# Kernel tuning notes

Measured on AMD Instinct MI355X. Metric: run time of the kernel, lower is better.

Reference implementation:

```python
import jax, jax.numpy as jnp
import numpy as np

B, T, D = 4, 2048, 1024
H = 16
DK = D // H


def setup_inputs() -> dict:
    key = jax.random.key(0)
    k1, k2, k3, k4 = jax.random.split(key, 4)
    x = jax.random.normal(k1, (B, T, D), dtype=jnp.float32)
    prefix_lengths = jax.random.randint(k2, (B,), 0, 1024, dtype=jnp.int64)
    # torch Linear weights: [out_features, in_features], scaled like kaiming-uniform-ish
    W_qkv = jax.random.normal(k3, (3 * D, D), dtype=jnp.float32) / np.sqrt(D)
    W_o = jax.random.normal(k4, (D, D), dtype=jnp.float32) / np.sqrt(D)
    return {"x": x, "prefix_lengths": prefix_lengths, "W_qkv": W_qkv, "W_o": W_o}


def _prefix_lm_mask(seq_len, prefix_lengths):
    # True where attention is BLOCKED.
    pos = jnp.arange(seq_len)
    key_pos = pos[None, None, :]          # [1,1,T]
    query_pos = pos[None, :, None]        # [1,T,1]
    prefix = prefix_lengths[:, None, None]  # [B,1,1]
    q_in_pre = query_pos < prefix
    k_in_pre = key_pos < prefix
    block_pre_to_suf = q_in_pre & ~k_in_pre
    block_future_suf = ~q_in_pre & ~k_in_pre & (key_pos > query_pos)
    return block_pre_to_suf | block_future_suf  # [B,T,T]


def reference(x, prefix_lengths, W_qkv, W_o):
    Bb, Tt, Cc = x.shape
    qkv = x @ W_qkv.T                     # [B,T,3D]
    qkv = qkv.reshape(Bb, Tt, 3, H, DK).transpose(2, 0, 3, 1, 4)  # [3,B,H,T,dk]
    q, k, v = qkv[0], qkv[1], qkv[2]
    scale = 1.0 / np.sqrt(DK).astype(np.float32)
    attn = jnp.einsum('bhqd,bhkd->bhqk', q, k) * scale  # [B,H,T,T]
    pl = jnp.clip(prefix_lengths.astype(jnp.int32), 0, Tt)
    mask = _prefix_lm_mask(Tt, pl)        # [B,T,T]
    attn = jnp.where(mask[:, None, :, :], -jnp.inf, attn)
    attn = jax.nn.softmax(attn, axis=-1)
    out = jnp.einsum('bhqk,bhkd->bhqd', attn, v)  # [B,H,T,dk]
    out = out.transpose(0, 2, 1, 3).reshape(Bb, Tt, Cc)
    return out @ W_o.T
```

## Files before the change

### kernel.cpp

```cpp
#include <hip/hip_runtime.h>
#include <stdint.h>

#define NB 4
#define NT 2048
#define ND 1024
#define NH 16
#define NDK 64
#define NTD 3072

typedef __attribute__((ext_vector_type(8))) short short8;
typedef __attribute__((ext_vector_type(4))) float f32x4;
typedef unsigned short u16;
typedef unsigned int u32;

__device__ __forceinline__ u16 f2bf(float f) {
    u32 u = __builtin_bit_cast(u32, f);
    u += 0x7fffu + ((u >> 16) & 1u);
    return (u16)(u >> 16);
}
__device__ __forceinline__ float bf2f(u16 s) {
    u32 u = ((u32)s) << 16;
    return __builtin_bit_cast(float, u);
}

__device__ __forceinline__ void gl_lds16(const u16* g, u16* l) {
    __builtin_amdgcn_global_load_lds(
        (const __attribute__((address_space(1))) u32*)g,
        (__attribute__((address_space(3))) u32*)l, 16, 0, 0);
}

__device__ __forceinline__ int swz(int row, int col) {
    return row * 32 + ((((col >> 3) ^ (row >> 1) ^ (row >> 3)) & 3) << 3) + (col & 7);
}

__global__ __launch_bounds__(256) void cvt_all(const float* __restrict__ x,
                                               const float* __restrict__ wqkv,
                                               const float* __restrict__ wo,
                                               u16* __restrict__ xb,
                                               u16* __restrict__ wqb,
                                               u16* __restrict__ wob) {
    const int n0 = NB * NT * ND;
    const int n1 = 3 * ND * ND;
    int i = (blockIdx.x * 256 + threadIdx.x) * 8;
    const float* src;
    u16* dst;
    if (i < n0) {
        src = x + i; dst = xb + i;
    } else if (i < n0 + n1) {
        src = wqkv + (i - n0); dst = wqb + (i - n0);
    } else {
        src = wo + (i - n0 - n1); dst = wob + (i - n0 - n1);
    }
    float4 a = *(const float4*)(src);
    float4 b = *(const float4*)(src + 4);
    short8 r;
    r[0] = (short)f2bf(a.x); r[1] = (short)f2bf(a.y);
    r[2] = (short)f2bf(a.z); r[3] = (short)f2bf(a.w);
    r[4] = (short)f2bf(b.x); r[5] = (short)f2bf(b.y);
    r[6] = (short)f2bf(b.z); r[7] = (short)f2bf(b.w);
    *(short8*)(dst) = r;
}

template <typename OutT>
__global__ __launch_bounds__(256) void gemm_bt(const u16* __restrict__ A,
                                               const u16* __restrict__ Bm,
                                               OutT* __restrict__ C,
                                               int M, int N, int K) {
    __shared__ __align__(16) u16 As[128 * 32];
    __shared__ __align__(16) u16 Bs[128 * 32];
    const int tid  = threadIdx.x;
    const int wave = tid >> 6, lane = tid & 63;
    const int quad = lane >> 4, l16 = lane & 15;
    const int wm = wave >> 1, wn = wave & 1;
    const int fid = blockIdx.y * gridDim.x + blockIdx.x;
    const int bx = ((fid & 7) << 3) | ((fid >> 3) & 7);
    const int by = fid >> 6;
    const int row0 = bx * 128, col0 = by * 128;

    f32x4 acc[4][4];
#pragma unroll
    for (int i = 0; i < 4; ++i)
#pragma unroll
        for (int j = 0; j < 4; ++j) acc[i][j] = (f32x4){0.f, 0.f, 0.f, 0.f};

    const u16* Ag = A + (size_t)(row0 + (tid >> 2)) * K + ((tid & 3) * 8);
    const u16* Bg = Bm + (size_t)(col0 + (tid >> 2)) * K + ((tid & 3) * 8);
    const size_t stride64 = (size_t)64 * K;
    u16* As0 = As + wave * 512;
    u16* As1 = As + 2048 + wave * 512;
    u16* Bs0 = Bs + wave * 512;
    u16* Bs1 = Bs + 2048 + wave * 512;

    for (int k0 = 0; k0 < K; k0 += 32) {
        gl_lds16(Ag + k0, As0);
        gl_lds16(Ag + k0 + stride64, As1);
        gl_lds16(Bg + k0, Bs0);
        gl_lds16(Bg + k0 + stride64, Bs1);
        __syncthreads();
        short8 af[4], bfr[4];
#pragma unroll
        for (int mi = 0; mi < 4; ++mi)
            af[mi] = *(const short8*)&As[(wm * 64 + mi * 16 + l16) * 32 + quad * 8];
#pragma unroll
        for (int ni = 0; ni < 4; ++ni)
            bfr[ni] = *(const short8*)&Bs[(wn * 64 + ni * 16 + l16) * 32 + quad * 8];
#pragma unroll
        for (int mi = 0; mi < 4; ++mi)
#pragma unroll
            for (int ni = 0; ni < 4; ++ni)
                acc[mi][ni] = __builtin_amdgcn_mfma_f32_16x16x32_bf16(
                    af[mi], bfr[ni], acc[mi][ni], 0, 0, 0);
        __syncthreads();
    }

#pragma unroll
    for (int mi = 0; mi < 4; ++mi) {
#pragma unroll
        for (int ni = 0; ni < 4; ++ni) {
            const int r = row0 + wm * 64 + mi * 16 + quad * 4;
            const int c = col0 + wn * 64 + ni * 16 + l16;
#pragma unroll
            for (int rr = 0; rr < 4; ++rr) {
                float v = acc[mi][ni][rr];
                if constexpr (sizeof(OutT) == 2)
                    C[(size_t)(r + rr) * N + c] = (OutT)f2bf(v);
                else
                    C[(size_t)(r + rr) * N + c] = (OutT)v;
            }
        }
    }
}

__global__ __launch_bounds__(256) void gemm_qkv(const u16* __restrict__ A,
                                                const u16* __restrict__ Bm,
                                                u16* __restrict__ Cq,
                                                u16* __restrict__ vtb) {
    const int Kd = ND, Nn = NTD;
    __shared__ __align__(16) u16 As[128 * 32];
    __shared__ __align__(16) u16 Bs[128 * 32];
    const int tid  = threadIdx.x;
    const int wave = tid >> 6, lane = tid & 63;
    const int quad = lane >> 4, l16 = lane & 15;
    const int wm = wave >> 1, wn = wave & 1;
    const int fid = blockIdx.y * gridDim.x + blockIdx.x;
    const int bx = ((fid & 7) << 3) | ((fid >> 3) & 7);
    const int by = fid >> 6;
    const int row0 = bx * 128, col0 = by * 128;

    f32x4 acc[4][4];
#pragma unroll
    for (int i = 0; i < 4; ++i)
#pragma unroll
        for (int j = 0; j < 4; ++j) acc[i][j] = (f32x4){0.f, 0.f, 0.f, 0.f};

    const u16* Ag = A + (size_t)(row0 + (tid >> 2)) * Kd + ((tid & 3) * 8);
    const u16* Bg = Bm + (size_t)(col0 + (tid >> 2)) * Kd + ((tid & 3) * 8);
    const size_t stride64 = (size_t)64 * Kd;
    u16* As0 = As + wave * 512;
    u16* As1 = As + 2048 + wave * 512;
    u16* Bs0 = Bs + wave * 512;
    u16* Bs1 = Bs + 2048 + wave * 512;

    for (int k0 = 0; k0 < Kd; k0 += 32) {
        gl_lds16(Ag + k0, As0);
        gl_lds16(Ag + k0 + stride64, As1);
        gl_lds16(Bg + k0, Bs0);
        gl_lds16(Bg + k0 + stride64, Bs1);
        __syncthreads();
        short8 af[4], bfr[4];
#pragma unroll
        for (int mi = 0; mi < 4; ++mi)
            af[mi] = *(const short8*)&As[(wm * 64 + mi * 16 + l16) * 32 + quad * 8];
#pragma unroll
        for (int ni = 0; ni < 4; ++ni)
            bfr[ni] = *(const short8*)&Bs[(wn * 64 + ni * 16 + l16) * 32 + quad * 8];
#pragma unroll
        for (int mi = 0; mi < 4; ++mi)
#pragma unroll
            for (int ni = 0; ni < 4; ++ni)
                acc[mi][ni] = __builtin_amdgcn_mfma_f32_16x16x32_bf16(
                    af[mi], bfr[ni], acc[mi][ni], 0, 0, 0);
        __syncthreads();
    }

    if (col0 < 2048) {
#pragma unroll
        for (int mi = 0; mi < 4; ++mi)
#pragma unroll
            for (int ni = 0; ni < 4; ++ni) {
                const int r = row0 + wm * 64 + mi * 16 + quad * 4;
                const int c = col0 + wn * 64 + ni * 16 + l16;
#pragma unroll
                for (int rr = 0; rr < 4; ++rr)
                    Cq[(size_t)(r + rr) * Nn + c] = f2bf(acc[mi][ni][rr]);
            }
    } else {
        const int hb = ((col0 - 2048) >> 6) + wn;
        const int bq = (row0 + wm * 64) >> 11;
        const int tb = (row0 + wm * 64) & 2047;
        u16* Ovt = vtb + (size_t)(bq * NH + hb) * 64 * NT + tb;
#pragma unroll
        for (int phase = 0; phase < 2; ++phase) {
            __syncthreads();
            if ((wave >> 1) == phase) {
                u16* L = (wave & 1) ? Bs : As;
#pragma unroll
                for (int mi = 0; mi < 4; ++mi) {
                    const int r4 = mi * 4 + quad;
#pragma unroll
                    for (int ni = 0; ni < 4; ++ni) {
                        const int cl = ni * 16 + l16;
                        u32 lo = (u32)f2bf(acc[mi][ni][0]) | ((u32)f2bf(acc[mi][ni][1]) << 16);
                        u32 hi = (u32)f2bf(acc[mi][ni][2]) | ((u32)f2bf(acc[mi][ni][3]) << 16);
                        u32* p = (u32*)&L[cl * 64 + (((r4 ^ cl) & 15) << 2)];
                        p[0] = lo; p[1] = hi;
                    }
                }
#pragma unroll
                for (int rep = 0; rep < 8; ++rep) {
                    const int cl = (lane >> 3) + rep * 8;
                    const int tc = lane & 7;
                    const u32* p0 = (const u32*)&L[cl * 64 + ((((2 * tc) ^ cl) & 15) << 2)];
                    const u32* p1 = (const u32*)&L[cl * 64 + ((((2 * tc + 1) ^ cl) & 15) << 2)];
                    u32 o0 = p0[0], o1 = p0[1], o2 = p1[0], o3 = p1[1];
                    u32* q = (u32*)(Ovt + (size_t)cl * NT + tc * 8);
                    q[0] = o0; q[1] = o1; q[2] = o2; q[3] = o3;
                }
            }
        }
    }
}

#define GETREG_XCC_ID 6164
__global__ __launch_bounds__(256) void flash_prefix(const u16* __restrict__ qkv,
                                                    const u16* __restrict__ vt,
                                                    const int* __restrict__ plen,
                                                    u16* __restrict__ attn,
                                                    u32* __restrict__ ctr) {
    __shared__ __align__(16) u16 Vt2[2][2048];
    __shared__ __align__(16) u16 Kt2[2][2048];
    __shared__ __align__(16) u16 Pl[4 * 512];
    __shared__ int taskS;

    const int tid  = threadIdx.x;
    const int wave = tid >> 6, lane = tid & 63;
    const int quad = lane >> 4, l16 = lane & 15;
    const float QSCALE = 0.18033688f;
    const int ldsoff = wave * 512;

    short8 ones;
#pragma unroll
    for (int j = 0; j < 8; ++j) ones[j] = (short)0x3F80;

    const bool is64 = (plen[1] == 0) && (plen[3] == 0);
    const int xcd = (int)(__builtin_amdgcn_s_getreg(GETREG_XCC_ID) & 7);
    int q = xcd;

    for (;;) {
        if (tid == 0) taskS = (int)atomicAdd(ctr + q * 16, 1u);
        __syncthreads();
        const int pos = taskS;
        if (pos >= 256) {
            q = (q + 1) & 7;
            if (q == xcd) break;
            continue;
        }

        const int bh = (q << 3) | (pos & 7);
        const int b = bh >> 4, h = bh & 15;
        const int q0 = (31 - (pos >> 3)) * 64;

        int P = is64 ? plen[2 * b] : plen[b];
        P = P < 0 ? 0 : (P > NT ? NT : P);

        const u16* Qg = qkv + (size_t)b * NT * NTD + h * NDK;
        const u16* Kg = Qg + ND;
        const u16* Vtb = vt + (size_t)bh * 64 * NT;
        const int qbase = q0 + wave * 16;
        u16* Pw = Pl + wave * 512;

        const int vrow = tid >> 2;
        const int vtq = (tid ^ (vrow >> 1) ^ (vrow >> 3)) & 3;
        const u16* vsrc = Vtb + (size_t)vrow * NT + vtq * 8;
        const int krow = tid >> 3;
        const int kc = (tid ^ krow) & 7;
        const u16* ksrc = Kg + (size_t)krow * NTD + kc * 8;

        short8 qa[2];
#pragma unroll
        for (int kd = 0; kd < 2; ++kd) {
            short8 tq = *(const short8*)(Qg + (size_t)(qbase + l16) * NTD + kd * 32 + quad * 8);
#pragma unroll
            for (int j = 0; j < 8; ++j)
                tq[j] = (short)f2bf(bf2f((u16)tq[j]) * QSCALE);
            qa[kd] = tq;
        }

        f32x4 o[4];
#pragma unroll
        for (int nt = 0; nt < 4; ++nt) o[nt] = (f32x4){0.f, 0.f, 0.f, 0.f};
        f32x4 lsum = (f32x4){0.f, 0.f, 0.f, 0.f};

        int kl[4];
#pragma unroll
        for (int rr = 0; rr < 4; ++rr) {
            const int qrow = qbase + quad * 4 + rr;
            kl[rr] = (qrow < P) ? P : (qrow + 1);
        }
        const int klmin = (qbase < P) ? P : (qbase + 1);
        const int kmax = (q0 + 64 > P) ? (q0 + 64) : P;

        gl_lds16(vsrc, &Vt2[0][ldsoff]);
        gl_lds16(ksrc, &Kt2[0][ldsoff]);
        int buf = 0;

        for (int k0 = 0; k0 < kmax; k0 += 32) {
            __syncthreads();
            if (k0 + 32 < kmax) {
                gl_lds16(vsrc + (k0 + 32), &Vt2[buf ^ 1][ldsoff]);
                gl_lds16(ksrc + (size_t)(k0 + 32) * NTD, &Kt2[buf ^ 1][ldsoff]);
            }
            const u16* Kb = Kt2[buf];
            const u16* Vb = Vt2[buf];

            f32x4 s[2];
#pragma unroll
            for (int ni = 0; ni < 2; ++ni) {
                s[ni] = (f32x4){0.f, 0.f, 0.f, 0.f};
#pragma unroll
                for (int kd = 0; kd < 2; ++kd) {
                    const int r = ni * 16 + l16;
                    const short8 kb = *(const short8*)&Kb[r * 64 + ((((kd * 4 + quad) ^ r) & 7) << 3)];
                    s[ni] = __builtin_amdgcn_mfma_f32_16x16x32_bf16(qa[kd], kb, s[ni], 0, 0, 0);
                }
            }

            const bool full = (k0 + 32 <= klmin);
#pragma unroll
            for (int ni = 0; ni < 2; ++ni) {
#pragma unroll
                for (int rr = 0; rr < 4; ++rr) {
                    float sv = s[ni][rr];
                    if (!full) {
                        const int kpos = k0 + ni * 16 + l16;
                        sv = (kpos < kl[rr]) ? sv : -1e30f;
                    }
                    const float p = exp2f(sv);
                    const u32 u = __builtin_bit_cast(u32, p) + 0x8000u;
                    Pw[swz(quad * 4 + rr, ni * 16 + l16)] = (u16)(u >> 16);
                }
            }

            const short8 pa = *(const short8*)&Pw[swz(l16, quad * 8)];
            lsum = __builtin_amdgcn_mfma_f32_16x16x32_bf16(pa, ones, lsum, 0, 0, 0);
#pragma unroll
            for (int nt = 0; nt < 4; ++nt) {
                const short8 vb = *(const short8*)&Vb[swz(nt * 16 + l16, quad * 8)];
                o[nt] = __builtin_amdgcn_mfma_f32_16x16x32_bf16(pa, vb, o[nt], 0, 0, 0);
            }
            buf ^= 1;
        }

#pragma unroll
        for (int rr = 0; rr < 4; ++rr) {
            const float inv = 1.0f / lsum[rr];
            const size_t rowoff = (size_t)(b * NT + qbase + quad * 4 + rr) * ND + h * NDK;
#pragma unroll
            for (int nt = 0; nt < 4; ++nt)
                attn[rowoff + nt * 16 + l16] = f2bf(o[nt][rr] * inv);
        }
    }
}

extern "C" void kernel_launch(void* const* d_in, const int* in_sizes, int n_in,
                              void* d_out, int out_size, void* d_ws, size_t ws_size,
                              hipStream_t stream) {
    const float* x    = (const float*)d_in[0];
    const int*   plen = (const int*)d_in[1];
    const float* wqkv = (const float*)d_in[2];
    const float* wo   = (const float*)d_in[3];
    float* out = (float*)d_out;

    char* ws = (char*)d_ws;
    u16* xb   = (u16*)(ws);
    u16* wqb  = (u16*)(ws + 16777216);
    u16* wob  = (u16*)(ws + 23068672);
    u16* qkv  = (u16*)(ws + 25165824);
    u16* attn = (u16*)(ws + 75497472);
    u16* vtb  = (u16*)(ws + 92274688);
    u32* ctr  = (u32*)(ws + 75496960);

    hipMemsetAsync(ctr, 0, 512, stream);

    cvt_all<<<6144, 256, 0, stream>>>(x, wqkv, wo, xb, wqb, wob);

    gemm_qkv<<<dim3(64, 24), 256, 0, stream>>>(xb, wqb, qkv, vtb);

    flash_prefix<<<1024, 256, 0, stream>>>(qkv, vtb, plen, attn, ctr);

    gemm_bt<float><<<dim3(64, 8), 256, 0, stream>>>(attn, wob, out, NB * NT, ND, ND);
}
```

Baseline: 297.8 us.

## Split QKV GEMM into 256x256 double-buffered QK kernel and separate V kernel

Splits the fused QKV projection in two. A new 512-thread kernel computes Q and K with 256x256 tiles, double-buffered LDS prefetch, XOR-swizzled LDS layout and MFMA priority hints. A separate 128x128 kernel computes V and writes it transposed. The larger tiles raise operand reuse and hide global load latency. The cost is an extra kernel launch and a smaller grid (256 blocks) for the QK part.

```diff
diff --git a/kernel.cpp b/kernel.cpp
--- a/kernel.cpp
+++ b/kernel.cpp
@@ -131,11 +131,119 @@
     }
 }
 
-__global__ __launch_bounds__(256) void gemm_qkv(const u16* __restrict__ A,
-                                                const u16* __restrict__ Bm,
-                                                u16* __restrict__ Cq,
-                                                u16* __restrict__ vtb) {
-    const int Kd = ND, Nn = NTD;
+__global__ __launch_bounds__(512, 2) void gemm_qk256(const u16* __restrict__ A,
+                                                     const u16* __restrict__ Bm,
+                                                     u16* __restrict__ Cq) {
+    __shared__ __align__(16) u16 rbA[2][8192];
+    __shared__ __align__(16) u16 rbB[2][8192];
+    u16* const rbAf = &rbA[0][0];
+    u16* const rbBf = &rbB[0][0];
+    const int tid  = threadIdx.x;
+    const int wave = tid >> 6, lane = tid & 63;
+    const int quad = lane >> 4, l16 = lane & 15;
+    const int wm = wave >> 2, wn = wave & 3;
+    const int K = ND;
+    const int fid = blockIdx.x;
+    const int bx = (fid & 7) * 4 + (fid >> 6);
+    const int by = (fid >> 3) & 7;
+    const int row0 = bx * 256, col0 = by * 256;
+
+    const int sr0 = tid >> 3, sl0 = (tid & 7) ^ (sr0 & 7);
+    const int a1 = 512 + tid;
+    const int sr1 = a1 >> 3, sl1 = (a1 & 7) ^ (sr1 & 7);
+    const int r0i = 2 * sr0 + (sl0 >> 2), k0i = (sl0 & 3) * 8;
+    const int r1i = 2 * sr1 + (sl1 >> 2), k1i = (sl1 & 3) * 8;
+    const u16* srcA0 = A + (size_t)(row0 + r0i) * K + k0i;
+    const u16* srcA1 = A + (size_t)(row0 + r1i) * K + k1i;
+    const u16* srcB0 = Bm + (size_t)(col0 + r0i) * K + k0i;
+    const u16* srcB1 = Bm + (size_t)(col0 + r1i) * K + k1i;
+    const int ldsc0 = wave * 512;
+    const int ldsc1 = 4096 + wave * 512;
+
+    int aoff[8], boff[4];
+#pragma unroll
+    for (int mi = 0; mi < 8; ++mi) {
+        const int row = wm * 128 + mi * 16 + l16;
+        const int srow = row >> 1;
+        const int slot = ((((row & 1) << 2) | quad) ^ (srow & 7));
+        aoff[mi] = srow * 64 + slot * 8;
+    }
+#pragma unroll
+    for (int ni = 0; ni < 4; ++ni) {
+        const int row = wn * 64 + ni * 16 + l16;
+        const int srow = row >> 1;
+        const int slot = ((((row & 1) << 2) | quad) ^ (srow & 7));
+        boff[ni] = srow * 64 + slot * 8;
+    }
+
+    f32x4 acc[8][4];
+#pragma unroll
+    for (int i = 0; i < 8; ++i)
+#pragma unroll
+        for (int j = 0; j < 4; ++j) acc[i][j] = (f32x4){0.f, 0.f, 0.f, 0.f};
+
+    gl_lds16(srcA0, rbAf + ldsc0);
+    gl_lds16(srcA1, rbAf + ldsc1);
+    gl_lds16(srcB0, rbBf + ldsc0);
+    gl_lds16(srcB1, rbBf + ldsc1);
+    __syncthreads();
+
+#define QK_TILE(T, TB, NB_)                                                    \
+    {                                                                          \
+        if ((T) + 1 < 32) {                                                    \
+            const int ko = ((T) + 1) * 32;                                     \
+            gl_lds16(srcA0 + ko, rbAf + (NB_) + ldsc0);                        \
+            gl_lds16(srcA1 + ko, rbAf + (NB_) + ldsc1);                        \
+            gl_lds16(srcB0 + ko, rbBf + (NB_) + ldsc0);                        \
+            gl_lds16(srcB1 + ko, rbBf + (NB_) + ldsc1);                        \
+        }                                                                      \
+        short8 af[4], bfr[4];                                                  \
+        _Pragma("unroll") for (int mi = 0; mi < 4; ++mi)                       \
+            af[mi] = *(const short8*)&rbAf[(TB) + aoff[mi]];                   \
+        _Pragma("unroll") for (int ni = 0; ni < 4; ++ni)                       \
+            bfr[ni] = *(const short8*)&rbBf[(TB) + boff[ni]];                  \
+        __builtin_amdgcn_s_setprio(1);                                         \
+        _Pragma("unroll") for (int mi = 0; mi < 4; ++mi)                       \
+            _Pragma("unroll") for (int ni = 0; ni < 4; ++ni)                   \
+                acc[mi][ni] = __builtin_amdgcn_mfma_f32_16x16x32_bf16(         \
+                    af[mi], bfr[ni], acc[mi][ni], 0, 0, 0);                    \
+        __builtin_amdgcn_s_setprio(0);                                         \
+        __builtin_amdgcn_s_barrier();                                          \
+        short8 af2[4];                                                         \
+        _Pragma("unroll") for (int mi = 0; mi < 4; ++mi)                       \
+            af2[mi] = *(const short8*)&rbAf[(TB) + aoff[4 + mi]];              \
+        __builtin_amdgcn_s_setprio(1);                                         \
+        _Pragma("unroll") for (int mi = 0; mi < 4; ++mi)                       \
+            _Pragma("unroll") for (int ni = 0; ni < 4; ++ni)                   \
+                acc[4 + mi][ni] = __builtin_amdgcn_mfma_f32_16x16x32_bf16(     \
+                    af2[mi], bfr[ni], acc[4 + mi][ni], 0, 0, 0);               \
+        __builtin_amdgcn_s_setprio(0);                                         \
+        __syncthreads();                                                       \
+    }
+
+    for (int t2 = 0; t2 < 32; t2 += 2) {
+        QK_TILE(t2, 0, 8192);
+        QK_TILE(t2 + 1, 8192, 0);
+    }
+#undef QK_TILE
+
+#pragma unroll
+    for (int mi = 0; mi < 8; ++mi) {
+#pragma unroll
+        for (int ni = 0; ni < 4; ++ni) {
+            const int r = row0 + wm * 128 + mi * 16 + quad * 4;
+            const int c = col0 + wn * 64 + ni * 16 + l16;
+#pragma unroll
+            for (int rr = 0; rr < 4; ++rr)
+                Cq[(size_t)(r + rr) * NTD + c] = f2bf(acc[mi][ni][rr]);
+        }
+    }
+}
+
+__global__ __launch_bounds__(256) void gemm_v(const u16* __restrict__ A,
+                                              const u16* __restrict__ Bm,
+                                              u16* __restrict__ vtb) {
+    const int Kd = ND;
     __shared__ __align__(16) u16 As[128 * 32];
     __shared__ __align__(16) u16 Bs[128 * 32];
     const int tid  = threadIdx.x;
@@ -145,7 +253,7 @@
     const int fid = blockIdx.y * gridDim.x + blockIdx.x;
     const int bx = ((fid & 7) << 3) | ((fid >> 3) & 7);
     const int by = fid >> 6;
-    const int row0 = bx * 128, col0 = by * 128;
+    const int row0 = bx * 128, col0 = 2048 + by * 128;
 
     f32x4 acc[4][4];
 #pragma unroll
@@ -183,49 +291,36 @@
         __syncthreads();
     }
 
-    if (col0 < 2048) {
-#pragma unroll
-        for (int mi = 0; mi < 4; ++mi)
-#pragma unroll
-            for (int ni = 0; ni < 4; ++ni) {
-                const int r = row0 + wm * 64 + mi * 16 + quad * 4;
-                const int c = col0 + wn * 64 + ni * 16 + l16;
-#pragma unroll
-                for (int rr = 0; rr < 4; ++rr)
-                    Cq[(size_t)(r + rr) * Nn + c] = f2bf(acc[mi][ni][rr]);
-            }
-    } else {
-        const int hb = ((col0 - 2048) >> 6) + wn;
-        const int bq = (row0 + wm * 64) >> 11;
-        const int tb = (row0 + wm * 64) & 2047;
-        u16* Ovt = vtb + (size_t)(bq * NH + hb) * 64 * NT + tb;
-#pragma unroll
-        for (int phase = 0; phase < 2; ++phase) {
-            __syncthreads();
-            if ((wave >> 1) == phase) {
-                u16* L = (wave & 1) ? Bs : As;
-#pragma unroll
-                for (int mi = 0; mi < 4; ++mi) {
-                    const int r4 = mi * 4 + quad;
-#pragma unroll
-                    for (int ni = 0; ni < 4; ++ni) {
-                        const int cl = ni * 16 + l16;
-                        u32 lo = (u32)f2bf(acc[mi][ni][0]) | ((u32)f2bf(acc[mi][ni][1]) << 16);
-                        u32 hi = (u32)f2bf(acc[mi][ni][2]) | ((u32)f2bf(acc[mi][ni][3]) << 16);
-                        u32* p = (u32*)&L[cl * 64 + (((r4 ^ cl) & 15) << 2)];
-                        p[0] = lo; p[1] = hi;
-                    }
+    const int hb = ((col0 - 2048) >> 6) + wn;
+    const int bq = (row0 + wm * 64) >> 11;
+    const int tb = (row0 + wm * 64) & 2047;
+    u16* Ovt = vtb + (size_t)(bq * NH + hb) * 64 * NT + tb;
+#pragma unroll
+    for (int phase = 0; phase < 2; ++phase) {
+        __syncthreads();
+        if ((wave >> 1) == phase) {
+            u16* L = (wave & 1) ? Bs : As;
+#pragma unroll
+            for (int mi = 0; mi < 4; ++mi) {
+                const int r4 = mi * 4 + quad;
+#pragma unroll
+                for (int ni = 0; ni < 4; ++ni) {
+                    const int cl = ni * 16 + l16;
+                    u32 lo = (u32)f2bf(acc[mi][ni][0]) | ((u32)f2bf(acc[mi][ni][1]) << 16);
+                    u32 hi = (u32)f2bf(acc[mi][ni][2]) | ((u32)f2bf(acc[mi][ni][3]) << 16);
+                    u32* p = (u32*)&L[cl * 64 + (((r4 ^ cl) & 15) << 2)];
+                    p[0] = lo; p[1] = hi;
                 }
-#pragma unroll
-                for (int rep = 0; rep < 8; ++rep) {
-                    const int cl = (lane >> 3) + rep * 8;
-                    const int tc = lane & 7;
-                    const u32* p0 = (const u32*)&L[cl * 64 + ((((2 * tc) ^ cl) & 15) << 2)];
-                    const u32* p1 = (const u32*)&L[cl * 64 + ((((2 * tc + 1) ^ cl) & 15) << 2)];
-                    u32 o0 = p0[0], o1 = p0[1], o2 = p1[0], o3 = p1[1];
-                    u32* q = (u32*)(Ovt + (size_t)cl * NT + tc * 8);
-                    q[0] = o0; q[1] = o1; q[2] = o2; q[3] = o3;
-                }
+            }
+#pragma unroll
+            for (int rep = 0; rep < 8; ++rep) {
+                const int cl = (lane >> 3) + rep * 8;
+                const int tc = lane & 7;
+                const u32* p0 = (const u32*)&L[cl * 64 + ((((2 * tc) ^ cl) & 15) << 2)];
+                const u32* p1 = (const u32*)&L[cl * 64 + ((((2 * tc + 1) ^ cl) & 15) << 2)];
+                u32 o0 = p0[0], o1 = p0[1], o2 = p1[0], o3 = p1[1];
+                u32* q = (u32*)(Ovt + (size_t)cl * NT + tc * 8);
+                q[0] = o0; q[1] = o1; q[2] = o2; q[3] = o3;
             }
         }
     }
@@ -394,7 +489,9 @@
 
     cvt_all<<<6144, 256, 0, stream>>>(x, wqkv, wo, xb, wqb, wob);
 
-    gemm_qkv<<<dim3(64, 24), 256, 0, stream>>>(xb, wqb, qkv, vtb);
+    gemm_qk256<<<256, 512, 0, stream>>>(xb, wqb, qkv);
+
+    gemm_v<<<dim3(64, 8), 256, 0, stream>>>(xb, wqb, vtb);
 
     flash_prefix<<<1024, 256, 0, stream>>>(qkv, vtb, plen, attn, ctr);
 
```

Measured after the change: 292.1 us (median of 2 runs). No clear change (-1.9%).
